# Kernel tuning notes

Hardware: AMD Instinct MI355X
Metric: run time of the kernel (lower is better)

## Reference

```python
import jax, jax.numpy as jnp
import numpy as np

N_NODES = 50000
N_EDGES = 800000
HIDDEN = 64
OUT = 16
N_LAYERS = 3


def setup_inputs() -> dict:
    key = jax.random.key(0)
    ks = jax.random.split(key, 8)
    s = 1.0 / np.sqrt(HIDDEN)
    x = jax.random.normal(ks[0], (N_NODES, HIDDEN), dtype=jnp.float32)
    edge_index = jax.random.randint(ks[1], (2, N_EDGES), 0, N_NODES, dtype=jnp.int64)
    # SAGEConv params per layer: lin_l (neighbor path, with bias), lin_r (root path, no bias)
    Wl = jax.random.uniform(ks[2], (N_LAYERS, HIDDEN, HIDDEN), jnp.float32, -s, s)
    bl = jax.random.uniform(ks[3], (N_LAYERS, HIDDEN), jnp.float32, -s, s)
    Wr = jax.random.uniform(ks[4], (N_LAYERS, HIDDEN, HIDDEN), jnp.float32, -s, s)
    W_out = jax.random.uniform(ks[5], (HIDDEN, OUT), jnp.float32, -s, s)
    b_out = jax.random.uniform(ks[6], (OUT,), jnp.float32, -s, s)
    return {"x": x, "edge_index": edge_index, "Wl": Wl, "bl": bl, "Wr": Wr,
            "W_out": W_out, "b_out": b_out}


def reference(x, edge_index, Wl, bl, Wr, W_out, b_out):
    n = x.shape[0]
    src, dst = edge_index[0], edge_index[1]
    # in-degree for mean aggregation (clamped to 1 to avoid div-by-zero)
    deg = jax.ops.segment_sum(jnp.ones((src.shape[0],), x.dtype), dst, num_segments=n)
    deg = jnp.maximum(deg, 1.0)[:, None]  # [N, 1]
    for l in range(N_LAYERS):
        msg = x[src]                                            # [E, H] gather
        agg = jax.ops.segment_sum(msg, dst, num_segments=n) / deg  # scatter-mean [N, H]
        # SAGEConv: lin_l(agg) + lin_r(x)  (lin_r has no bias)
        x = agg @ Wl[l] + bl[l] + x @ Wr[l]
        x = jax.nn.relu(x)
    return x @ W_out + b_out
```

## Files before the change

kernel.cpp:

```cpp
#include <hip/hip_runtime.h>
#include <hip/hip_bf16.h>

#define NN 50000
#define NE 800000
#define HD 64
#define OD 16
#define CAP 64
#define TILES 3125
#define AST 72
#define SCATB 2048
#define PSZ 6250

typedef unsigned short u16;
typedef unsigned int u32;
typedef __attribute__((ext_vector_type(8))) short short8;
typedef __attribute__((ext_vector_type(4))) float f32x4;

__device__ __forceinline__ float bf2f(u16 v) { return __uint_as_float(((u32)v) << 16); }
__device__ __forceinline__ u16 f2bf(float f) {
  __hip_bfloat16 h = __float2bfloat16(f);
  return *reinterpret_cast<u16*>(&h);
}
__device__ __forceinline__ float ldf(const void* p, long i, bool f32m) {
  return f32m ? ((const float*)p)[i] : bf2f(((const u16*)p)[i]);
}
__device__ __forceinline__ int edge_at(const void* eidx, long pos, bool i64) {
  return i64 ? (int)((const long long*)eidx)[pos] : ((const int*)eidx)[pos];
}

__device__ __forceinline__ bool detect_i64(const u32* e32, int lane) {
  return __ballot(e32[2 * lane + 1] != 0u) == 0ull;
}
__device__ __forceinline__ bool detect_f32(const u32* x32, int lane) {
  u32 v = x32[lane] & 0xffffu;
  int e = (int)((v >> 7) & 0xff);
  bool wild = (v != 0u) && (e < 100 || e > 140);
  return __popcll(__ballot(wild)) > 16;
}

__global__ __launch_bounds__(256) void k_pre(
    const void* __restrict__ x, const void* __restrict__ eidx,
    const void* __restrict__ Wl, const void* __restrict__ bl,
    const void* __restrict__ Wr, const void* __restrict__ Wo,
    const void* __restrict__ bo,
    int* __restrict__ deg, u16* __restrict__ csr, u32* __restrict__ spill,
    u16* __restrict__ xA, u16* __restrict__ wfrag, u16* __restrict__ pfrag,
    float* __restrict__ blf, float* __restrict__ bof,
    int* __restrict__ flags) {
  int lane = threadIdx.x & 63;
  if (blockIdx.x < SCATB) {
    bool i64 = detect_i64((const u32*)eidx, lane);
    int g = blockIdx.x & 7;
    int lo = g * PSZ, hi = lo + PSZ;
    int base = (blockIdx.x >> 3) * 256 + threadIdx.x;
    for (int e = base; e < NE; e += 65536) {
      int dst = edge_at(eidx, (long)NE + e, i64);
      if (dst >= lo && dst < hi) {
        int src = edge_at(eidx, e, i64);
        int pos = atomicAdd(&deg[dst], 1);
        if (pos < CAP) csr[(long)dst * CAP + pos] = (u16)src;
        else {
          int sp = atomicAdd(&flags[4], 1);
          spill[sp] = (u32)dst * 50000u + (u32)src;
        }
      }
    }
  } else {
    bool f32m = detect_f32((const u32*)x, lane);
    int i = (blockIdx.x - SCATB) * 256 + threadIdx.x;
    if (f32m) {
      float4 v = ((const float4*)x)[i];
      u32 lo = (u32)f2bf(v.x) | ((u32)f2bf(v.y) << 16);
      u32 hi = (u32)f2bf(v.z) | ((u32)f2bf(v.w) << 16);
      ((u32*)xA)[2 * i] = lo;
      ((u32*)xA)[2 * i + 1] = hi;
    }
    if (i < 3 * 16 * 64 * 8) {
      int j = i & 7, ln = (i >> 3) & 63, f = (i >> 9) & 15, l = i >> 13;
      int s = f >> 2, c = f & 3;
      int k = 32 * s + ((ln >> 4) << 3) + j;
      int n = (c << 4) + (ln & 15);
      long wbase = (long)l * HD * HD;
      float v = (k < HD) ? ldf(Wl, wbase + (long)k * HD + n, f32m)
                         : ldf(Wr, wbase + (long)(k - HD) * HD + n, f32m);
      wfrag[i] = f2bf(v);
    }
    if (i < 2 * 64 * 8) {
      int j = i & 7, ln = (i >> 3) & 63, s = i >> 9;
      int k = 32 * s + ((ln >> 4) << 3) + j;
      pfrag[i] = f2bf(ldf(Wo, (long)k * OD + (ln & 15), f32m));
    }
    if (i < 3 * HD) blf[i] = ldf(bl, i, f32m);
    if (i < OD) bof[i] = ldf(bo, i, f32m);
  }
}

__global__ __launch_bounds__(256, 8) void k_fused(
    const u16* __restrict__ xin_bf, const u16* __restrict__ xin_f32m,
    const u32* __restrict__ xorig32, u16* __restrict__ xout,
    const int* __restrict__ deg, const u16* __restrict__ csr,
    const u32* __restrict__ spill,
    const u16* __restrict__ wfrag, const u16* __restrict__ pfrag,
    const float* __restrict__ bl3, const float* __restrict__ bof,
    void* __restrict__ outp, int layer, int doProj,
    const int* __restrict__ flags) {
  __shared__ __align__(16) u16 aw[16 * AST];
  __shared__ float sbl[HD];
  __shared__ float sbo[OD];
  if (threadIdx.x < HD) sbl[threadIdx.x] = bl3[layer * HD + threadIdx.x];
  if (threadIdx.x < OD) sbo[threadIdx.x] = bof[threadIdx.x];
  int lane = threadIdx.x & 63;
  bool f32m = detect_f32(xorig32, lane);
  int spillcnt = __builtin_amdgcn_readfirstlane(flags[4]);
  const u16* xin = f32m ? xin_f32m : xin_bf;
  const u32* x32 = (const u32*)xin;

  int w = threadIdx.x >> 6;
  int nb = blockIdx.x * 16;
  int n0 = nb + 4 * w;
  int grp = lane >> 4;
  int f = lane & 15;
  u32* aw32 = (u32*)aw;

  int4 dv = *(const int4*)(deg + n0);
  int dt[4] = {__builtin_amdgcn_readfirstlane(dv.x),
               __builtin_amdgcn_readfirstlane(dv.y),
               __builtin_amdgcn_readfirstlane(dv.z),
               __builtin_amdgcn_readfirstlane(dv.w)};
  int idx[4];
#pragma unroll
  for (int g = 0; g < 4; ++g) {
    int d = dt[g] < CAP ? dt[g] : CAP;
    idx[g] = (lane < d) ? (int)csr[(long)(n0 + g) * CAP + lane] : 0;
  }

#pragma unroll
  for (int ph = 0; ph < 2; ++ph) {
    const u32* xph = x32 + ph * 16;
#pragma unroll
    for (int gp = 0; gp < 4; gp += 2) {
      int dA = dt[gp] < CAP ? dt[gp] : CAP;
      int dB = dt[gp + 1] < CAP ? dt[gp + 1] : CAP;
      int dmax = dA > dB ? dA : dB;
      float alo = 0.f, ahi = 0.f, blo = 0.f, bhi = 0.f;
      for (int j = 0; j < dmax; j += 16) {
        u32 va[4], vb[4];
#pragma unroll
        for (int p = 0; p < 4; ++p) {
          int sa = __shfl(idx[gp], j + 4 * p + grp);
          int sb = __shfl(idx[gp + 1], j + 4 * p + grp);
          va[p] = xph[(long)sa * 32 + f];
          vb[p] = xph[(long)sb * 32 + f];
        }
#pragma unroll
        for (int p = 0; p < 4; ++p) {
          int m = j + 4 * p + grp;
          u32 a = (m < dA) ? va[p] : 0u;
          u32 b = (m < dB) ? vb[p] : 0u;
          alo += __uint_as_float(a << 16);
          ahi += __uint_as_float(a & 0xffff0000u);
          blo += __uint_as_float(b << 16);
          bhi += __uint_as_float(b & 0xffff0000u);
        }
      }
      alo += __shfl_xor(alo, 16); ahi += __shfl_xor(ahi, 16);
      blo += __shfl_xor(blo, 16); bhi += __shfl_xor(bhi, 16);
      alo += __shfl_xor(alo, 32); ahi += __shfl_xor(ahi, 32);
      blo += __shfl_xor(blo, 32); bhi += __shfl_xor(bhi, 32);
      if (spillcnt > 0) {
#pragma unroll
        for (int q = 0; q < 2; ++q) {
          int n = n0 + gp + q;
          for (int base = 0; base < spillcnt; base += 64) {
            u32 p = (base + lane < spillcnt) ? spill[base + lane] : 0xffffffffu;
            u32 dd = p / 50000u;
            u32 ss = p - dd * 50000u;
            unsigned long long mk = __ballot(dd == (u32)n);
            while (mk) {
              int jj = __builtin_ctzll(mk);
              mk &= mk - 1;
              int s = __builtin_amdgcn_readlane((int)ss, jj);
              u32 v = xph[(long)s * 32 + f];
              float vlo = __uint_as_float(v << 16);
              float vhi = __uint_as_float(v & 0xffff0000u);
              if (q) { blo += vlo; bhi += vhi; }
              else   { alo += vlo; ahi += vhi; }
            }
          }
        }
      }
      if (lane < 16) {
        float rdA = 1.0f / (float)(dt[gp] > 0 ? dt[gp] : 1);
        float rdB = 1.0f / (float)(dt[gp + 1] > 0 ? dt[gp + 1] : 1);
        aw32[(4 * w + gp) * (AST / 2) + ph * 16 + f] =
            (u32)f2bf(alo * rdA) | ((u32)f2bf(ahi * rdA) << 16);
        aw32[(4 * w + gp + 1) * (AST / 2) + ph * 16 + f] =
            (u32)f2bf(blo * rdB) | ((u32)f2bf(bhi * rdB) << 16);
      }
    }
  }
  __syncthreads();

  int quad = lane >> 4, m16 = lane & 15;
  short8 a0 = *(const short8*)(aw + m16 * AST + quad * 8);
  short8 a1 = *(const short8*)(aw + m16 * AST + 32 + quad * 8);
  const u16* xrow = xin + (long)(nb + m16) * HD;
  short8 x2 = *(const short8*)(xrow + quad * 8);
  short8 x3 = *(const short8*)(xrow + 32 + quad * 8);
  int c = w;
  const short8* bp = (const short8*)(wfrag + (long)layer * 16 * 64 * 8);
  short8 b0 = bp[(0 * 4 + c) * 64 + lane];
  short8 b1 = bp[(1 * 4 + c) * 64 + lane];
  short8 b2 = bp[(2 * 4 + c) * 64 + lane];
  short8 b3 = bp[(3 * 4 + c) * 64 + lane];
  float bb = sbl[c * 16 + m16];
  f32x4 acc = (f32x4){bb, bb, bb, bb};
  acc = __builtin_amdgcn_mfma_f32_16x16x32_bf16(a0, b0, acc, 0, 0, 0);
  acc = __builtin_amdgcn_mfma_f32_16x16x32_bf16(a1, b1, acc, 0, 0, 0);
  acc = __builtin_amdgcn_mfma_f32_16x16x32_bf16(x2, b2, acc, 0, 0, 0);
  acc = __builtin_amdgcn_mfma_f32_16x16x32_bf16(x3, b3, acc, 0, 0, 0);
  __syncthreads();

#pragma unroll
  for (int r = 0; r < 4; ++r)
    aw[(quad * 4 + r) * AST + c * 16 + m16] = f2bf(fmaxf(acc[r], 0.f));
  __syncthreads();

  if (!doProj) {
    int row = threadIdx.x >> 4, ch = threadIdx.x & 15;
    uint2 v = *(const uint2*)(aw + row * AST + ch * 4);
    *(uint2*)(xout + (long)(nb + row) * HD + ch * 4) = v;
  } else if (w == 0) {
    short8 pa0 = *(const short8*)(aw + m16 * AST + quad * 8);
    short8 pa1 = *(const short8*)(aw + m16 * AST + 32 + quad * 8);
    const short8* pb = (const short8*)pfrag;
    short8 pb0 = pb[lane];
    short8 pb1 = pb[64 + lane];
    float bv = sbo[m16];
    f32x4 pacc = (f32x4){bv, bv, bv, bv};
    pacc = __builtin_amdgcn_mfma_f32_16x16x32_bf16(pa0, pb0, pacc, 0, 0, 0);
    pacc = __builtin_amdgcn_mfma_f32_16x16x32_bf16(pa1, pb1, pacc, 0, 0, 0);
    if (f32m) {
      float* o = (float*)outp;
#pragma unroll
      for (int r = 0; r < 4; ++r)
        o[(long)(nb + quad * 4 + r) * OD + m16] = pacc[r];
    } else {
      u16* o = (u16*)outp;
#pragma unroll
      for (int r = 0; r < 4; ++r)
        o[(long)(nb + quad * 4 + r) * OD + m16] = f2bf(pacc[r]);
    }
  }
}

extern "C" void kernel_launch(void* const* d_in, const int* in_sizes, int n_in,
                              void* d_out, int out_size, void* d_ws, size_t ws_size,
                              hipStream_t stream) {
  const void* x = d_in[0];
  const void* eidx = d_in[1];
  const void* Wl = d_in[2];
  const void* bl = d_in[3];
  const void* Wr = d_in[4];
  const void* Wo = d_in[5];
  const void* bo = d_in[6];

  char* w = (char*)d_ws;
  size_t off = 0;
  int* flags = (int*)(w + off);     off += 256;
  int* deg = (int*)(w + off);       off += (size_t)NN * 4 + 192;
  size_t memset_bytes = off;
  u16* csr = (u16*)(w + off);       off += (size_t)NN * CAP * 2;
  u32* spill = (u32*)(w + off);     off += (size_t)NE * 4;
  u16* wfrag = (u16*)(w + off);     off += 3 * 16 * 64 * 8 * 2;
  u16* pfrag = (u16*)(w + off);     off += 2 * 64 * 8 * 2;
  float* blf = (float*)(w + off);   off += 3 * HD * 4;
  float* bof = (float*)(w + off);   off += 256;
  u16* xA = (u16*)(w + off);        off += (size_t)NN * HD * 2;
  u16* xB = (u16*)(w + off);        off += (size_t)NN * HD * 2;

  hipMemsetAsync(flags, 0, memset_bytes, stream);

  k_pre<<<SCATB + 3125, 256, 0, stream>>>(x, eidx, Wl, bl, Wr, Wo, bo,
                                          deg, csr, spill, xA, wfrag, pfrag,
                                          blf, bof, flags);

  const u32* xo32 = (const u32*)x;
  k_fused<<<TILES, 256, 0, stream>>>((const u16*)x, xA, xo32, xB, deg, csr, spill,
                                     wfrag, pfrag, blf, bof, (void*)0, 0, 0, flags);
  k_fused<<<TILES, 256, 0, stream>>>(xB, xB, xo32, xA, deg, csr, spill,
                                     wfrag, pfrag, blf, bof, (void*)0, 1, 0, flags);
  k_fused<<<TILES, 256, 0, stream>>>(xA, xA, xo32, (u16*)0, deg, csr, spill,
                                     wfrag, pfrag, blf, bof, d_out, 2, 1, flags);
}
```

Before: 190.0 us.

## Split each layer's gather into two feature-half kernels for better cache locality

Each fused layer kernel becomes two launches. The first gathers and averages the low 32 features of the neighbours into a packed bf16 buffer in global memory. The second gathers the high 32 features, reads the low half back and runs the MFMA update. Gathering one half at a time halves the working set of the random gather, so more of it can stay in L2/MALL, and each wave now handles four nodes at once for more memory-level parallelism. Nontemporal loads and stores are added for streaming data. The cost is three extra kernel launches, an extra round trip through global memory for the aggregate buffer, and a second pass over the CSR lists.

```diff
diff --git a/kernel.cpp b/kernel.cpp
--- a/kernel.cpp
+++ b/kernel.cpp
@@ -15,6 +15,7 @@
 typedef unsigned int u32;
 typedef __attribute__((ext_vector_type(8))) short short8;
 typedef __attribute__((ext_vector_type(4))) float f32x4;
+typedef __attribute__((ext_vector_type(2))) unsigned int u32x2;
 
 __device__ __forceinline__ float bf2f(u16 v) { return __uint_as_float(((u32)v) << 16); }
 __device__ __forceinline__ u16 f2bf(float f) {
@@ -95,9 +96,104 @@
   }
 }
 
-__global__ __launch_bounds__(256, 8) void k_fused(
+__device__ __forceinline__ void gather4(
+    const u32* __restrict__ xph, const u32* __restrict__ spill, int spillcnt,
+    const int* dt, const int* idx, int n0, int lane, int grp, int f,
+    float* slo, float* shi) {
+  int d[4], dmax = 0;
+#pragma unroll
+  for (int g = 0; g < 4; ++g) {
+    d[g] = dt[g] < CAP ? dt[g] : CAP;
+    if (d[g] > dmax) dmax = d[g];
+  }
+  float l0[4] = {0.f, 0.f, 0.f, 0.f}, h0[4] = {0.f, 0.f, 0.f, 0.f};
+  for (int j = 0; j < dmax; j += 16) {
+    u32 v[4][4];
+#pragma unroll
+    for (int jj = 0; jj < 4; ++jj)
+#pragma unroll
+      for (int g = 0; g < 4; ++g) {
+        int s = __shfl(idx[g], j + 4 * jj + grp);
+        v[jj][g] = xph[(long)s * 32 + f];
+      }
+#pragma unroll
+    for (int jj = 0; jj < 4; ++jj)
+#pragma unroll
+      for (int g = 0; g < 4; ++g) {
+        int m = j + 4 * jj + grp;
+        u32 vv = (m < d[g]) ? v[jj][g] : 0u;
+        l0[g] += __uint_as_float(vv << 16);
+        h0[g] += __uint_as_float(vv & 0xffff0000u);
+      }
+  }
+#pragma unroll
+  for (int g = 0; g < 4; ++g) {
+    float lo = l0[g], hi = h0[g];
+    lo += __shfl_xor(lo, 16); hi += __shfl_xor(hi, 16);
+    lo += __shfl_xor(lo, 32); hi += __shfl_xor(hi, 32);
+    if (spillcnt > 0) {
+      int n = n0 + g;
+      for (int base = 0; base < spillcnt; base += 64) {
+        u32 p = (base + lane < spillcnt) ? spill[base + lane] : 0xffffffffu;
+        u32 dd = p / 50000u;
+        u32 ss = p - dd * 50000u;
+        unsigned long long mk = __ballot(dd == (u32)n);
+        while (mk) {
+          int jj = __builtin_ctzll(mk);
+          mk &= mk - 1;
+          int s = __builtin_amdgcn_readlane((int)ss, jj);
+          u32 v = xph[(long)s * 32 + f];
+          lo += __uint_as_float(v << 16);
+          hi += __uint_as_float(v & 0xffff0000u);
+        }
+      }
+    }
+    slo[g] = lo; shi[g] = hi;
+  }
+}
+
+__global__ __launch_bounds__(256, 8) void k_gA(
     const u16* __restrict__ xin_bf, const u16* __restrict__ xin_f32m,
-    const u32* __restrict__ xorig32, u16* __restrict__ xout,
+    const u32* __restrict__ xorig32,
+    const int* __restrict__ deg, const u16* __restrict__ csr,
+    const u32* __restrict__ spill, u32* __restrict__ aggA,
+    const int* __restrict__ flags) {
+  int lane = threadIdx.x & 63;
+  bool f32m = detect_f32(xorig32, lane);
+  const u32* x32 = (const u32*)(f32m ? xin_f32m : xin_bf);
+  int spillcnt = __builtin_amdgcn_readfirstlane(flags[4]);
+  int w = threadIdx.x >> 6;
+  int n0 = blockIdx.x * 16 + 4 * w;
+  int grp = lane >> 4, f = lane & 15;
+
+  int4 dv = *(const int4*)(deg + n0);
+  int dt[4] = {__builtin_amdgcn_readfirstlane(dv.x),
+               __builtin_amdgcn_readfirstlane(dv.y),
+               __builtin_amdgcn_readfirstlane(dv.z),
+               __builtin_amdgcn_readfirstlane(dv.w)};
+  int idx[4];
+#pragma unroll
+  for (int g = 0; g < 4; ++g) {
+    int d = dt[g] < CAP ? dt[g] : CAP;
+    idx[g] = (lane < d)
+        ? (int)__builtin_nontemporal_load(csr + (long)(n0 + g) * CAP + lane) : 0;
+  }
+  float slo[4], shi[4];
+  gather4(x32, spill, spillcnt, dt, idx, n0, lane, grp, f, slo, shi);
+  if (lane < 16) {
+#pragma unroll
+    for (int g = 0; g < 4; ++g) {
+      float rd = 1.0f / (float)(dt[g] > 0 ? dt[g] : 1);
+      u32 pk = (u32)f2bf(slo[g] * rd) | ((u32)f2bf(shi[g] * rd) << 16);
+      __builtin_nontemporal_store(pk, aggA + (long)(n0 + g) * 16 + f);
+    }
+  }
+}
+
+__global__ __launch_bounds__(256, 8) void k_gB(
+    const u16* __restrict__ xin_bf, const u16* __restrict__ xin_f32m,
+    const u32* __restrict__ xorig32, const u32* __restrict__ aggA,
+    u16* __restrict__ xout,
     const int* __restrict__ deg, const u16* __restrict__ csr,
     const u32* __restrict__ spill,
     const u16* __restrict__ wfrag, const u16* __restrict__ pfrag,
@@ -118,8 +214,7 @@
   int w = threadIdx.x >> 6;
   int nb = blockIdx.x * 16;
   int n0 = nb + 4 * w;
-  int grp = lane >> 4;
-  int f = lane & 15;
+  int grp = lane >> 4, f = lane & 15;
   u32* aw32 = (u32*)aw;
 
   int4 dv = *(const int4*)(deg + n0);
@@ -131,82 +226,28 @@
 #pragma unroll
   for (int g = 0; g < 4; ++g) {
     int d = dt[g] < CAP ? dt[g] : CAP;
-    idx[g] = (lane < d) ? (int)csr[(long)(n0 + g) * CAP + lane] : 0;
-  }
-
-#pragma unroll
-  for (int ph = 0; ph < 2; ++ph) {
-    const u32* xph = x32 + ph * 16;
-#pragma unroll
-    for (int gp = 0; gp < 4; gp += 2) {
-      int dA = dt[gp] < CAP ? dt[gp] : CAP;
-      int dB = dt[gp + 1] < CAP ? dt[gp + 1] : CAP;
-      int dmax = dA > dB ? dA : dB;
-      float alo = 0.f, ahi = 0.f, blo = 0.f, bhi = 0.f;
-      for (int j = 0; j < dmax; j += 16) {
-        u32 va[4], vb[4];
-#pragma unroll
-        for (int p = 0; p < 4; ++p) {
-          int sa = __shfl(idx[gp], j + 4 * p + grp);
-          int sb = __shfl(idx[gp + 1], j + 4 * p + grp);
-          va[p] = xph[(long)sa * 32 + f];
-          vb[p] = xph[(long)sb * 32 + f];
-        }
-#pragma unroll
-        for (int p = 0; p < 4; ++p) {
-          int m = j + 4 * p + grp;
-          u32 a = (m < dA) ? va[p] : 0u;
-          u32 b = (m < dB) ? vb[p] : 0u;
-          alo += __uint_as_float(a << 16);
-          ahi += __uint_as_float(a & 0xffff0000u);
-          blo += __uint_as_float(b << 16);
-          bhi += __uint_as_float(b & 0xffff0000u);
-        }
-      }
-      alo += __shfl_xor(alo, 16); ahi += __shfl_xor(ahi, 16);
-      blo += __shfl_xor(blo, 16); bhi += __shfl_xor(bhi, 16);
-      alo += __shfl_xor(alo, 32); ahi += __shfl_xor(ahi, 32);
-      blo += __shfl_xor(blo, 32); bhi += __shfl_xor(bhi, 32);
-      if (spillcnt > 0) {
-#pragma unroll
-        for (int q = 0; q < 2; ++q) {
-          int n = n0 + gp + q;
-          for (int base = 0; base < spillcnt; base += 64) {
-            u32 p = (base + lane < spillcnt) ? spill[base + lane] : 0xffffffffu;
-            u32 dd = p / 50000u;
-            u32 ss = p - dd * 50000u;
-            unsigned long long mk = __ballot(dd == (u32)n);
-            while (mk) {
-              int jj = __builtin_ctzll(mk);
-              mk &= mk - 1;
-              int s = __builtin_amdgcn_readlane((int)ss, jj);
-              u32 v = xph[(long)s * 32 + f];
-              float vlo = __uint_as_float(v << 16);
-              float vhi = __uint_as_float(v & 0xffff0000u);
-              if (q) { blo += vlo; bhi += vhi; }
-              else   { alo += vlo; ahi += vhi; }
-            }
-          }
-        }
-      }
-      if (lane < 16) {
-        float rdA = 1.0f / (float)(dt[gp] > 0 ? dt[gp] : 1);
-        float rdB = 1.0f / (float)(dt[gp + 1] > 0 ? dt[gp + 1] : 1);
-        aw32[(4 * w + gp) * (AST / 2) + ph * 16 + f] =
-            (u32)f2bf(alo * rdA) | ((u32)f2bf(ahi * rdA) << 16);
-        aw32[(4 * w + gp + 1) * (AST / 2) + ph * 16 + f] =
-            (u32)f2bf(blo * rdB) | ((u32)f2bf(bhi * rdB) << 16);
-      }
+    idx[g] = (lane < d)
+        ? (int)__builtin_nontemporal_load(csr + (long)(n0 + g) * CAP + lane) : 0;
+  }
+  float slo[4], shi[4];
+  gather4(x32 + 16, spill, spillcnt, dt, idx, n0, lane, grp, f, slo, shi);
+  if (lane < 16) {
+#pragma unroll
+    for (int g = 0; g < 4; ++g) {
+      float rd = 1.0f / (float)(dt[g] > 0 ? dt[g] : 1);
+      aw32[(4 * w + g) * (AST / 2) + 16 + f] =
+          (u32)f2bf(slo[g] * rd) | ((u32)f2bf(shi[g] * rd) << 16);
     }
   }
   __syncthreads();
 
   int quad = lane >> 4, m16 = lane & 15;
-  short8 a0 = *(const short8*)(aw + m16 * AST + quad * 8);
+  short8 a0 = __builtin_nontemporal_load(
+      (const short8*)(aggA + (long)(nb + m16) * 16 + quad * 4));
   short8 a1 = *(const short8*)(aw + m16 * AST + 32 + quad * 8);
-  const u16* xrow = xin + (long)(nb + m16) * HD;
-  short8 x2 = *(const short8*)(xrow + quad * 8);
-  short8 x3 = *(const short8*)(xrow + 32 + quad * 8);
+  const short8* xr = (const short8*)(xin + (long)(nb + m16) * HD);
+  short8 x2 = __builtin_nontemporal_load(xr + quad);
+  short8 x3 = __builtin_nontemporal_load(xr + 4 + quad);
   int c = w;
   const short8* bp = (const short8*)(wfrag + (long)layer * 16 * 64 * 8);
   short8 b0 = bp[(0 * 4 + c) * 64 + lane];
@@ -228,8 +269,8 @@
 
   if (!doProj) {
     int row = threadIdx.x >> 4, ch = threadIdx.x & 15;
-    uint2 v = *(const uint2*)(aw + row * AST + ch * 4);
-    *(uint2*)(xout + (long)(nb + row) * HD + ch * 4) = v;
+    u32x2 v = *(const u32x2*)(aw + row * AST + ch * 4);
+    __builtin_nontemporal_store(v, (u32x2*)(xout + (long)(nb + row) * HD + ch * 4));
   } else if (w == 0) {
     short8 pa0 = *(const short8*)(aw + m16 * AST + quad * 8);
     short8 pa1 = *(const short8*)(aw + m16 * AST + 32 + quad * 8);
@@ -272,6 +313,7 @@
   size_t memset_bytes = off;
   u16* csr = (u16*)(w + off);       off += (size_t)NN * CAP * 2;
   u32* spill = (u32*)(w + off);     off += (size_t)NE * 4;
+  u32* aggA = (u32*)(w + off);      off += (size_t)NN * 16 * 4;
   u16* wfrag = (u16*)(w + off);     off += 3 * 16 * 64 * 8 * 2;
   u16* pfrag = (u16*)(w + off);     off += 2 * 64 * 8 * 2;
   float* blf = (float*)(w + off);   off += 3 * HD * 4;
@@ -286,10 +328,14 @@
                                           blf, bof, flags);
 
   const u32* xo32 = (const u32*)x;
-  k_fused<<<TILES, 256, 0, stream>>>((const u16*)x, xA, xo32, xB, deg, csr, spill,
-                                     wfrag, pfrag, blf, bof, (void*)0, 0, 0, flags);
-  k_fused<<<TILES, 256, 0, stream>>>(xB, xB, xo32, xA, deg, csr, spill,
-                                     wfrag, pfrag, blf, bof, (void*)0, 1, 0, flags);
-  k_fused<<<TILES, 256, 0, stream>>>(xA, xA, xo32, (u16*)0, deg, csr, spill,
-                                     wfrag, pfrag, blf, bof, d_out, 2, 1, flags);
-}
+  const u16* x16 = (const u16*)x;
+  k_gA<<<TILES, 256, 0, stream>>>(x16, xA, xo32, deg, csr, spill, aggA, flags);
+  k_gB<<<TILES, 256, 0, stream>>>(x16, xA, xo32, aggA, xB, deg, csr, spill,
+                                  wfrag, pfrag, blf, bof, (void*)0, 0, 0, flags);
+  k_gA<<<TILES, 256, 0, stream>>>(xB, xB, xo32, deg, csr, spill, aggA, flags);
+  k_gB<<<TILES, 256, 0, stream>>>(xB, xB, xo32, aggA, xA, deg, csr, spill,
+                                  wfrag, pfrag, blf, bof, (void*)0, 1, 0, flags);
+  k_gA<<<TILES, 256, 0, stream>>>(xA, xA, xo32, deg, csr, spill, aggA, flags);
+  k_gB<<<TILES, 256, 0, stream>>>(xA, xA, xo32, aggA, (u16*)0, deg, csr, spill,
+                                  wfrag, pfrag, blf, bof, d_out, 2, 1, flags);
+}
```

Result: slower. 228.7 us (+20.4%).
